# Optimization experiments

Hardware: AMD Instinct MI355X
Metric: run time of the kernel (lower is better)

## Reference

```python
import jax, jax.numpy as jnp
import numpy as np

B, D, H, W, C = 2, 6, 64, 64, 192
NH = 8                      # num heads
HD = C // NH                # head dim
E, K, HID = 8, 2, 384       # experts, top_k, d_hidden
WS = (2, 8, 8)              # window size (Wd, Wh, Ww)
SS = (1, 4, 4)              # shift size
N = WS[0] * WS[1] * WS[2]   # 128 tokens per window
NW = (D // WS[0]) * (H // WS[1]) * (W // WS[2])  # 192 windows per sample
SCALE = HD ** -0.5


def _rel_pos_index():
    coords = np.stack(np.meshgrid(np.arange(WS[0]), np.arange(WS[1]), np.arange(WS[2]), indexing='ij'))
    coords = coords.reshape(3, -1)
    rel = (coords[:, :, None] - coords[:, None, :]).transpose(1, 2, 0).astype(np.int64)
    rel[..., 0] += WS[0] - 1
    rel[..., 1] += WS[1] - 1
    rel[..., 2] += WS[2] - 1
    rel[..., 0] *= (2 * WS[1] - 1) * (2 * WS[2] - 1)
    rel[..., 1] *= (2 * WS[2] - 1)
    return rel.sum(-1)  # (N, N)


def _sine_pos_encoding():
    # VRT get_sine_position_encoding(window_size[1:], dim//2, normalize=True)
    h, w, nf = WS[1], WS[2], C // 2
    scale = 2 * np.pi
    y = np.cumsum(np.ones((1, h, w)), 1)
    x = np.cumsum(np.ones((1, h, w)), 2)
    y = y / (y[:, -1:, :] + 1e-6) * scale
    x = x / (x[:, :, -1:] + 1e-6) * scale
    dim_t = 10000.0 ** (2 * (np.arange(nf) // 2) / nf)
    px = x[..., None] / dim_t
    py = y[..., None] / dim_t
    px = np.stack([np.sin(px[..., 0::2]), np.cos(px[..., 1::2])], -1).reshape(1, h, w, -1)
    py = np.stack([np.sin(py[..., 0::2]), np.cos(py[..., 1::2])], -1).reshape(1, h, w, -1)
    return np.concatenate([py, px], -1).reshape(1, h * w, C).astype(np.float32)


def _compute_mask():
    # VRT compute_mask for cyclic shift
    img = np.zeros((1, D, H, W, 1))
    cnt = 0
    for d in (slice(0, -WS[0]), slice(-WS[0], -SS[0]), slice(-SS[0], None)):
        for h in (slice(0, -WS[1]), slice(-WS[1], -SS[1]), slice(-SS[1], None)):
            for w in (slice(0, -WS[2]), slice(-WS[2], -SS[2]), slice(-SS[2], None)):
                img[:, d, h, w, :] = cnt
                cnt += 1
    mw = img.reshape(1, D // WS[0], WS[0], H // WS[1], WS[1], W // WS[2], WS[2], 1)
    mw = mw.transpose(0, 1, 3, 5, 2, 4, 6, 7).reshape(-1, N)
    am = mw[:, None, :] - mw[:, :, None]
    return np.where(am != 0, -100.0, 0.0).astype(np.float32)  # (NW, N, N)


RP_INDEX = jnp.asarray(_rel_pos_index())
POS_BIAS = jnp.asarray(_sine_pos_encoding())  # (1, Wh*Ww, C)


def layernorm(x, w, b):
    mu = x.mean(-1, keepdims=True)
    var = ((x - mu) ** 2).mean(-1, keepdims=True)
    return (x - mu) * jax.lax.rsqrt(var + 1e-5) * w + b


def window_partition(x):
    x = x.reshape(B, D // WS[0], WS[0], H // WS[1], WS[1], W // WS[2], WS[2], C)
    return x.transpose(0, 1, 3, 5, 2, 4, 6, 7).reshape(-1, N, C)


def window_reverse(wx):
    x = wx.reshape(B, D // WS[0], H // WS[1], W // WS[2], WS[0], WS[1], WS[2], C)
    return x.transpose(0, 1, 4, 2, 5, 3, 6, 7).reshape(B, D, H, W, C)


def _attn(q, k, v, mask, bias):
    # q,k,v: (B_, NH, n, HD); mask: (NW, N, N) or None; bias: (NH, n, n) or None
    n = q.shape[2]
    a = jnp.einsum('bhnd,bhmd->bhnm', q * SCALE, k)
    if bias is not None:
        a = a + bias[None]
    if mask is not None:
        a = a.reshape(-1, NW, NH, n, n) + mask[None, :, None, :n, :n]
        a = a.reshape(-1, NH, n, n)
    a = jax.nn.softmax(a, -1)
    o = jnp.einsum('bhnm,bhmd->bhnd', a, v)
    return o.transpose(0, 2, 1, 3).reshape(o.shape[0], n, NH * HD)


def reference(x, mask_matrix, n1_w, n1_b, qkv_self_w, qkv_self_b, qkv_mut_w, qkv_mut_b,
              rpb_table, proj_w, proj_b, n2_w, n2_b, gate_w, gate_b, W1, b1, W2, b2):
    # ---- part 1: shifted 3D window attention (self + mutual) ----
    xn = layernorm(x, n1_w, n1_b)
    xs = jnp.roll(xn, shift=(-SS[0], -SS[1], -SS[2]), axis=(1, 2, 3))
    xw = window_partition(xs)  # (B_, N, C)
    B_ = xw.shape[0]

    def qkv_split(t):
        t = t.reshape(B_, -1, 3, NH, HD).transpose(2, 0, 3, 1, 4)
        return t[0], t[1], t[2]

    # self attention with relative position bias
    q, k, v = qkv_split(xw @ qkv_self_w + qkv_self_b)
    bias = rpb_table[RP_INDEX.reshape(-1)].reshape(N, N, NH).transpose(2, 0, 1)
    x_self = _attn(q, k, v, mask_matrix, bias)

    # mutual attention between the two frames of each window
    xm = xw + jnp.tile(POS_BIAS, (1, 2, 1))
    q, k, v = qkv_split(xm @ qkv_mut_w + qkv_mut_b)
    half = N // 2
    q1, q2 = q[:, :, :half], q[:, :, half:]
    k1, k2 = k[:, :, :half], k[:, :, half:]
    v1, v2 = v[:, :, :half], v[:, :, half:]
    x1 = _attn(q2, k1, v1, mask_matrix, None)
    x2 = _attn(q1, k2, v2, mask_matrix, None)
    x_out = jnp.concatenate([jnp.concatenate([x1, x2], 1), x_self], 2)  # (B_, N, 2C)

    attn_out = x_out @ proj_w + proj_b  # (B_, N, C)
    xr = window_reverse(attn_out)
    xr = jnp.roll(xr, shift=SS, axis=(1, 2, 3))
    x = x + xr

    # ---- part 2: MoE FFN (top-2 gate, per-expert 2-layer MLP, weighted combine) ----
    xn = layernorm(x, n2_w, n2_b).reshape(-1, C)  # (T, C)
    logits = xn @ gate_w + gate_b  # (T, E)
    top_val, top_idx = jax.lax.top_k(logits, K)
    scores = jax.nn.softmax(top_val, -1)  # (T, K)
    cw = (jax.nn.one_hot(top_idx, E, dtype=xn.dtype) * scores[..., None]).sum(1)  # (T, E)

    def body(acc, p):
        w1, bb1, w2, bb2, cwe = p
        hdd = jax.nn.gelu(xn @ w1 + bb1, approximate=False)
        return acc + cwe[:, None] * (hdd @ w2 + bb2), None

    moe_out, _ = jax.lax.scan(body, jnp.zeros_like(xn), (W1, b1, W2, b2, cw.T))
    return x + moe_out.reshape(B, D, H, W, C)


def setup_inputs() -> dict:
    key = jax.random.key(0)
    ks = jax.random.split(key, 8)
    s = 0.02
    tbl = (2 * WS[0] - 1) * (2 * WS[1] - 1) * (2 * WS[2] - 1)
    return dict(
        x=jax.random.normal(ks[0], (B, D, H, W, C), jnp.float32),
        mask_matrix=jnp.asarray(_compute_mask()),
        n1_w=jnp.ones((C,), jnp.float32), n1_b=jnp.zeros((C,), jnp.float32),
        qkv_self_w=jax.random.normal(ks[1], (C, 3 * C), jnp.float32) * s,
        qkv_self_b=jnp.zeros((3 * C,), jnp.float32),
        qkv_mut_w=jax.random.normal(ks[2], (C, 3 * C), jnp.float32) * s,
        qkv_mut_b=jnp.zeros((3 * C,), jnp.float32),
        rpb_table=jax.random.normal(ks[3], (tbl, NH), jnp.float32) * s,
        proj_w=jax.random.normal(ks[4], (2 * C, C), jnp.float32) * s,
        proj_b=jnp.zeros((C,), jnp.float32),
        n2_w=jnp.ones((C,), jnp.float32), n2_b=jnp.zeros((C,), jnp.float32),
        gate_w=jax.random.normal(ks[5], (C, E), jnp.float32) * s,
        gate_b=jnp.zeros((E,), jnp.float32),
        W1=jax.random.normal(ks[6], (E, C, HID), jnp.float32) * s,
        b1=jnp.zeros((E, HID), jnp.float32),
        W2=jax.random.normal(ks[7], (E, HID, C), jnp.float32) * s,
        b2=jnp.zeros((E, C), jnp.float32),
    )
```

## Files before the change

kernel.cpp:

```cpp
#include <hip/hip_runtime.h>
#include <hip/hip_bf16.h>

#define NW_ 192
#define NWIN 384
#define NTOK 128
#define CC 192
#define NHD 8
#define HD 24
#define QKVC 576
#define NROWS 49152
#define HIDN 384
#define SCALE_Q 0.20412414523193154f

typedef __hip_bfloat16 bf16;
typedef __attribute__((ext_vector_type(8))) short s16x8;
typedef __attribute__((ext_vector_type(4))) float f32x4;

__device__ __forceinline__ float waveRedSum(float v) {
    v += __shfl_xor(v, 32);
    v += __shfl_xor(v, 16);
    v += __shfl_xor(v, 8);
    v += __shfl_xor(v, 4);
    v += __shfl_xor(v, 2);
    v += __shfl_xor(v, 1);
    return v;
}

__device__ __forceinline__ size_t row_to_x(int r) {
    int wb = r >> 7;
    int n = r & 127;
    int b = wb / NW_;
    int rem = wb % NW_;
    int wd = rem >> 6;
    int wh = (rem >> 3) & 7;
    int ww = rem & 7;
    int id = n >> 6;
    int ih = (n >> 3) & 7;
    int iw = n & 7;
    int d = (wd * 2 + id + 1) % 6;
    int h = (wh * 8 + ih + 4) & 63;
    int w = (ww * 8 + iw + 4) & 63;
    return ((size_t)((b * 6 + d) * 64 + h) * 64 + w) * CC;
}

__device__ __forceinline__ void split_store(float v, bf16* hi, bf16* lo) {
    bf16 h = __float2bfloat16(v);
    *hi = h;
    *lo = __float2bfloat16(v - __bfloat162float(h));
}

__global__ void zero_counts(int* counts) {
    if (threadIdx.x < 8) counts[threadIdx.x] = 0;
}

__global__ __launch_bounds__(256) void transpose_w(
    const float* __restrict__ in, bf16* __restrict__ out_hi,
    bf16* __restrict__ out_lo, int K, int N) {
    size_t total = (size_t)K * N;
    in += (size_t)blockIdx.z * total;
    out_hi += (size_t)blockIdx.z * total;
    int t = blockIdx.x * 256 + threadIdx.x;
    if (t >= (int)total) return;
    int n = t / K, k = t % K;
    float v = in[(size_t)k * N + n];
    bf16 h = __float2bfloat16(v);
    out_hi[t] = h;
    if (out_lo) {
        out_lo += (size_t)blockIdx.z * total;
        out_lo[t] = __float2bfloat16(v - __bfloat162float(h));
    }
}

__global__ __launch_bounds__(256) void build_rpbx(
    const float* __restrict__ rpb, float* __restrict__ rpbx) {
    int idx = blockIdx.x * 256 + threadIdx.x;
    int q = idx >> 7, k = idx & 127;
    int dn = q >> 6, hn = (q >> 3) & 7, wn = q & 7;
    int dm = k >> 6, hm = (k >> 3) & 7, wm = k & 7;
    int ridx = (dn - dm + 1) * 225 + (hn - hm + 7) * 15 + (wn - wm + 7);
#pragma unroll
    for (int h = 0; h < 8; ++h)
        rpbx[h * 16384 + idx] = rpb[ridx * 8 + h];
}

__global__ __launch_bounds__(256) void ln1_partition(
    const float* __restrict__ x, const float* __restrict__ n1w,
    const float* __restrict__ n1b, bf16* __restrict__ xw_hi,
    bf16* __restrict__ xw_lo) {
    int r = blockIdx.x * 4 + (threadIdx.x >> 6);
    int t = threadIdx.x & 63;
    const float* src = x + row_to_x(r);
    float v0 = src[t], v1 = src[t + 64], v2 = src[t + 128];
    float mu = waveRedSum(v0 + v1 + v2) * (1.0f / 192.0f);
    float d0 = v0 - mu, d1 = v1 - mu, d2 = v2 - mu;
    float var = waveRedSum(d0 * d0 + d1 * d1 + d2 * d2) * (1.0f / 192.0f);
    float rstd = rsqrtf(var + 1e-5f);
    size_t b = (size_t)r * CC;
    split_store(d0 * rstd * n1w[t]       + n1b[t],       xw_hi + b + t,       xw_lo + b + t);
    split_store(d1 * rstd * n1w[t + 64]  + n1b[t + 64],  xw_hi + b + t + 64,  xw_lo + b + t + 64);
    split_store(d2 * rstd * n1w[t + 128] + n1b[t + 128], xw_hi + b + t + 128, xw_lo + b + t + 128);
}

__global__ __launch_bounds__(256) void add_posbias(
    bf16* __restrict__ hi, bf16* __restrict__ lo) {
    int idx = blockIdx.x * 256 + threadIdx.x;
    if (idx >= NROWS * CC) return;
    int c = idx % CC;
    int r = idx / CC;
    int n = r & 127;
    int tkn = n & 63;
    int h = tkn >> 3, w = tkn & 7;
    const float twopi_over = 6.283185307179586f / (8.0f + 1e-6f);
    float coord = (c < 96) ? (h + 1) * twopi_over : (w + 1) * twopi_over;
    int cc = (c < 96) ? c : c - 96;
    int j = cc >> 1;
    float v = coord * __expf(-0.1918820910968785f * (float)j);
    float pe = (cc & 1) ? __cosf(v) : __sinf(v);
    float val = __bfloat162float(hi[idx]) + __bfloat162float(lo[idx]) + pe;
    split_store(val, hi + idx, lo + idx);
}

template <int EPI, int GSHIFT, bool GATHER, bool SPLIT>
__global__ __launch_bounds__(256) void mgemm(
    const bf16* __restrict__ A, const bf16* __restrict__ Alo, int ldA,
    const bf16* __restrict__ Wt, const bf16* __restrict__ Wtlo, int wStrideE,
    const float* __restrict__ bias, int biasStrideE,
    float* __restrict__ Cf, bf16* __restrict__ Cb,
    int M, int K, int N,
    const int* __restrict__ counts, const int* __restrict__ lists,
    const float* __restrict__ wts, const float* __restrict__ xres) {
    int e = blockIdx.z;
    int Mq = counts ? counts[e] : M;
    int bm = blockIdx.x * 64;
    if (bm >= Mq) return;
    int bn = blockIdx.y * 64;
    const int lbase = e * NROWS;
    __shared__ __align__(16) bf16 As[64][72];
    __shared__ __align__(16) bf16 Bs[64][72];
    __shared__ __align__(16) bf16 Asl[(SPLIT ? 64 : 1)][72];
    __shared__ __align__(16) bf16 Bsl[(SPLIT ? 64 : 1)][72];
    int t = threadIdx.x;
    int trow = t >> 2, tko = (t & 3) * 8;
    size_t aoff;
    if (GATHER) {
        int p = bm + trow;
        int a = lists[lbase + (p < Mq ? p : 0)];
        aoff = (size_t)(a >> GSHIFT) * (size_t)ldA + tko;
    } else {
        aoff = (size_t)(bm + trow) * (size_t)ldA + tko;
    }
    size_t boff = (size_t)e * wStrideE + (size_t)(bn + trow) * K + tko;
    int wv = t >> 6, l = t & 63;
    int fr = l & 15, fg = l >> 4;
    f32x4 acc[4] = {{0.f,0.f,0.f,0.f},{0.f,0.f,0.f,0.f},
                    {0.f,0.f,0.f,0.f},{0.f,0.f,0.f,0.f}};
    for (int k0 = 0; k0 < K; k0 += 64) {
        __syncthreads();
        *(int4*)&As[trow][tko]      = *(const int4*)(A + aoff + k0);
        *(int4*)&As[trow][tko + 32] = *(const int4*)(A + aoff + k0 + 32);
        *(int4*)&Bs[trow][tko]      = *(const int4*)(Wt + boff + k0);
        *(int4*)&Bs[trow][tko + 32] = *(const int4*)(Wt + boff + k0 + 32);
        if (SPLIT) {
            *(int4*)&Asl[trow][tko]      = *(const int4*)(Alo + aoff + k0);
            *(int4*)&Asl[trow][tko + 32] = *(const int4*)(Alo + aoff + k0 + 32);
            *(int4*)&Bsl[trow][tko]      = *(const int4*)(Wtlo + boff + k0);
            *(int4*)&Bsl[trow][tko + 32] = *(const int4*)(Wtlo + boff + k0 + 32);
        }
        __syncthreads();
#pragma unroll
        for (int ks = 0; ks < 2; ++ks) {
            s16x8 ah = *(const s16x8*)&As[wv * 16 + fr][ks * 32 + fg * 8];
            s16x8 al;
            if (SPLIT) al = *(const s16x8*)&Asl[wv * 16 + fr][ks * 32 + fg * 8];
#pragma unroll
            for (int nt = 0; nt < 4; ++nt) {
                s16x8 bh = *(const s16x8*)&Bs[nt * 16 + fr][ks * 32 + fg * 8];
                acc[nt] = __builtin_amdgcn_mfma_f32_16x16x32_bf16(ah, bh, acc[nt], 0, 0, 0);
                if (SPLIT) {
                    s16x8 bl = *(const s16x8*)&Bsl[nt * 16 + fr][ks * 32 + fg * 8];
                    acc[nt] = __builtin_amdgcn_mfma_f32_16x16x32_bf16(ah, bl, acc[nt], 0, 0, 0);
                    acc[nt] = __builtin_amdgcn_mfma_f32_16x16x32_bf16(al, bh, acc[nt], 0, 0, 0);
                }
            }
        }
    }
    int row0 = bm + wv * 16 + fg * 4;
    if (EPI == 0) {
#pragma unroll
        for (int nt = 0; nt < 4; ++nt) {
            int c = bn + nt * 16 + fr;
            float bv = bias[c];
#pragma unroll
            for (int i = 0; i < 4; ++i)
                Cf[(size_t)(row0 + i) * N + c] = acc[nt][i] + bv;
        }
    } else if (EPI == 1) {
        size_t sr[4];
#pragma unroll
        for (int i = 0; i < 4; ++i) sr[i] = row_to_x(row0 + i);
#pragma unroll
        for (int nt = 0; nt < 4; ++nt) {
            int c = bn + nt * 16 + fr;
            float bv = bias[c];
#pragma unroll
            for (int i = 0; i < 4; ++i)
                Cf[sr[i] + c] = xres[sr[i] + c] + acc[nt][i] + bv;
        }
    } else if (EPI == 2) {
        const float* bp = bias + (size_t)e * biasStrideE;
#pragma unroll
        for (int i = 0; i < 4; ++i) {
            int p = row0 + i;
            if (p < Mq) {
                int a = lists[lbase + p];
#pragma unroll
                for (int nt = 0; nt < 4; ++nt) {
                    int c = bn + nt * 16 + fr;
                    float v = acc[nt][i] + bp[c];
                    float g = 0.5f * v * (1.0f + erff(v * 0.7071067811865476f));
                    Cb[(size_t)a * HIDN + c] = __float2bfloat16(g);
                }
            }
        }
    } else if (EPI == 3) {
        const float* bp = bias + (size_t)e * biasStrideE;
#pragma unroll
        for (int i = 0; i < 4; ++i) {
            int p = row0 + i;
            if (p < Mq) {
                int a = lists[lbase + p];
                int r = a >> 1;
                float w = wts[lbase + p];
#pragma unroll
                for (int nt = 0; nt < 4; ++nt) {
                    int c = bn + nt * 16 + fr;
                    atomicAdd(&Cf[(size_t)r * CC + c], w * (acc[nt][i] + bp[c]));
                }
            }
        }
    } else {
        const size_t S0 = (size_t)NROWS * 192;
        const size_t S1 = (size_t)NROWS * 24;
#pragma unroll
        for (int nt = 0; nt < 4; ++nt) {
            int c = bn + nt * 16 + fr;
            int which = c / 192;
            int rem = c - which * 192;
            int hh = rem / 24;
            int d = rem - hh * 24;
            float bv = bias[c];
            bf16* hb = Cb + (size_t)(2 * which) * S0 + (size_t)hh * S1;
            bf16* lb = Cb + (size_t)(2 * which + 1) * S0 + (size_t)hh * S1;
#pragma unroll
            for (int i = 0; i < 4; ++i) {
                float v = acc[nt][i] + bv;
                if (which == 0) v *= SCALE_Q;
                size_t o = (size_t)(row0 + i) * 24 + d;
                split_store(v, hb + o, lb + o);
            }
        }
    }
}

template <bool SELF>
__global__ __launch_bounds__(256) void attn_mfma(
    const bf16* __restrict__ qkvp, const float* __restrict__ mask,
    const float* __restrict__ rpbx, bf16* __restrict__ cat_hi,
    bf16* __restrict__ cat_lo) {
    constexpr int NT = SELF ? 128 : 64;
    constexpr int KT = NT / 16;
    constexpr int CPW = NT / 64;
    constexpr int KS = NT / 32;
    const size_t S0 = (size_t)NROWS * 192;
    const size_t S1 = (size_t)NROWS * 24;

    int wb = blockIdx.x, hh = blockIdx.y;
    int hf = SELF ? 0 : blockIdx.z;
    int qbase = wb * NTOK + (SELF ? 0 : (hf ? 0 : 64));
    int kvbase = wb * NTOK + (SELF ? 0 : (hf ? 64 : 0));
    int t = threadIdx.x;
    int wv = t >> 6, l = t & 63, fr = l & 15, fg = l >> 4;

    __shared__ __align__(16) ushort Vth[32][144];
    __shared__ __align__(16) ushort Vtl[32][144];
    __shared__ float linv_s[NT];

    {
        constexpr int PPT = 256 / NT;
        constexpr int DP = 24 / PPT;
        int tok = t % NT;
        int part = t / NT;
        const ushort* vh = (const ushort*)(qkvp + 4 * S0) + hh * S1 +
                           (size_t)(kvbase + tok) * 24 + part * DP;
        const ushort* vl = (const ushort*)(qkvp + 5 * S0) + hh * S1 +
                           (size_t)(kvbase + tok) * 24 + part * DP;
#pragma unroll
        for (int u = 0; u < DP; ++u) {
            Vth[part * DP + u][tok] = vh[u];
            Vtl[part * DP + u][tok] = vl[u];
        }
    }

    s16x8 zf = {0, 0, 0, 0, 0, 0, 0, 0};
    f32x4 st[KT][CPW];
#pragma unroll
    for (int kt = 0; kt < KT; ++kt)
#pragma unroll
        for (int c = 0; c < CPW; ++c) st[kt][c] = (f32x4){0.f, 0.f, 0.f, 0.f};

    s16x8 qfh[CPW], qfl[CPW];
#pragma unroll
    for (int c = 0; c < CPW; ++c) {
        int qt = wv * CPW + c;
        const bf16* qrow = qkvp + hh * S1 + (size_t)(qbase + qt * 16 + fr) * 24 + fg * 8;
        qfh[c] = (fg < 3) ? *(const s16x8*)qrow : zf;
        qfl[c] = (fg < 3) ? *(const s16x8*)(qrow + S0) : zf;
    }
#pragma unroll
    for (int kt = 0; kt < KT; ++kt) {
        const bf16* krow = qkvp + 2 * S0 + hh * S1 + (size_t)(kvbase + kt * 16 + fr) * 24 + fg * 8;
        s16x8 kh = (fg < 3) ? *(const s16x8*)krow : zf;
        s16x8 kl = (fg < 3) ? *(const s16x8*)(krow + S0) : zf;
#pragma unroll
        for (int c = 0; c < CPW; ++c) {
            st[kt][c] = __builtin_amdgcn_mfma_f32_16x16x32_bf16(kh, qfh[c], st[kt][c], 0, 0, 0);
            st[kt][c] = __builtin_amdgcn_mfma_f32_16x16x32_bf16(kh, qfl[c], st[kt][c], 0, 0, 0);
            st[kt][c] = __builtin_amdgcn_mfma_f32_16x16x32_bf16(kl, qfh[c], st[kt][c], 0, 0, 0);
        }
    }

    uint phq[KT][CPW][2], plq[KT][CPW][2];
#pragma unroll
    for (int c = 0; c < CPW; ++c) {
        int q = (wv * CPW + c) * 16 + fr;
        const float* mrow = mask + ((size_t)(wb % NW_) * NTOK + q) * NTOK;
        const float* brow = rpbx + ((size_t)hh * NTOK + q) * NTOK;
        float mx = -1e30f;
#pragma unroll
        for (int kt = 0; kt < KT; ++kt) {
            int k0 = kt * 16 + fg * 4;
            float4 mk = *(const float4*)(mrow + k0);
            if (SELF) {
                float4 bs = *(const float4*)(brow + k0);
                mk.x += bs.x; mk.y += bs.y; mk.z += bs.z; mk.w += bs.w;
            }
            st[kt][c][0] += mk.x; st[kt][c][1] += mk.y;
            st[kt][c][2] += mk.z; st[kt][c][3] += mk.w;
#pragma unroll
            for (int i = 0; i < 4; ++i) mx = fmaxf(mx, st[kt][c][i]);
        }
        mx = fmaxf(mx, __shfl_xor(mx, 16));
        mx = fmaxf(mx, __shfl_xor(mx, 32));
        float ls = 0.f;
#pragma unroll
        for (int kt = 0; kt < KT; ++kt)
#pragma unroll
            for (int i = 0; i < 4; ++i) {
                float pv = __expf(st[kt][c][i] - mx);
                st[kt][c][i] = pv;
                ls += pv;
            }
        ls += __shfl_xor(ls, 16);
        ls += __shfl_xor(ls, 32);
        if (fg == 0) linv_s[q] = 1.0f / ls;
#pragma unroll
        for (int kt = 0; kt < KT; ++kt) {
            ushort hb[4], lb[4];
#pragma unroll
            for (int i = 0; i < 4; ++i) {
                float pv = st[kt][c][i];
                bf16 ph = __float2bfloat16(pv);
                hb[i] = *(ushort*)&ph;
                bf16 pl = __float2bfloat16(pv - __bfloat162float(ph));
                lb[i] = *(ushort*)&pl;
            }
            phq[kt][c][0] = (uint)hb[0] | ((uint)hb[1] << 16);
            phq[kt][c][1] = (uint)hb[2] | ((uint)hb[3] << 16);
            plq[kt][c][0] = (uint)lb[0] | ((uint)lb[1] << 16);
            plq[kt][c][1] = (uint)lb[2] | ((uint)lb[3] << 16);
        }
    }
    __syncthreads();

    f32x4 oacc[CPW][2];
#pragma unroll
    for (int rt = 0; rt < CPW; ++rt)
#pragma unroll
        for (int ct = 0; ct < 2; ++ct) oacc[rt][ct] = (f32x4){0.f, 0.f, 0.f, 0.f};

    int sA = fr + 32 * (fg & 1);
    int sB = sA + 16;
    bool tsel = fg >= 2;
#pragma unroll
    for (int ks = 0; ks < KS; ++ks) {
        s16x8 bh[2], bl[2];
#pragma unroll
        for (int ct = 0; ct < 2; ++ct) {
            bh[ct] = *(const s16x8*)&Vth[ct * 16 + fr][ks * 32 + fg * 8];
            bl[ct] = *(const s16x8*)&Vtl[ct * 16 + fr][ks * 32 + fg * 8];
        }
#pragma unroll
        for (int rt = 0; rt < CPW; ++rt) {
            union { uint u[4]; s16x8 v; } ah, al;
            uint x0, x1;
            x0 = __shfl(phq[2 * ks][rt][0], sA); x1 = __shfl(phq[2 * ks + 1][rt][0], sA);
            ah.u[0] = tsel ? x1 : x0;
            x0 = __shfl(phq[2 * ks][rt][1], sA); x1 = __shfl(phq[2 * ks + 1][rt][1], sA);
            ah.u[1] = tsel ? x1 : x0;
            x0 = __shfl(phq[2 * ks][rt][0], sB); x1 = __shfl(phq[2 * ks + 1][rt][0], sB);
            ah.u[2] = tsel ? x1 : x0;
            x0 = __shfl(phq[2 * ks][rt][1], sB); x1 = __shfl(phq[2 * ks + 1][rt][1], sB);
            ah.u[3] = tsel ? x1 : x0;
            x0 = __shfl(plq[2 * ks][rt][0], sA); x1 = __shfl(plq[2 * ks + 1][rt][0], sA);
            al.u[0] = tsel ? x1 : x0;
            x0 = __shfl(plq[2 * ks][rt][1], sA); x1 = __shfl(plq[2 * ks + 1][rt][1], sA);
            al.u[1] = tsel ? x1 : x0;
            x0 = __shfl(plq[2 * ks][rt][0], sB); x1 = __shfl(plq[2 * ks + 1][rt][0], sB);
            al.u[2] = tsel ? x1 : x0;
            x0 = __shfl(plq[2 * ks][rt][1], sB); x1 = __shfl(plq[2 * ks + 1][rt][1], sB);
            al.u[3] = tsel ? x1 : x0;
#pragma unroll
            for (int ct = 0; ct < 2; ++ct) {
                oacc[rt][ct] = __builtin_amdgcn_mfma_f32_16x16x32_bf16(ah.v, bh[ct], oacc[rt][ct], 0, 0, 0);
                oacc[rt][ct] = __builtin_amdgcn_mfma_f32_16x16x32_bf16(ah.v, bl[ct], oacc[rt][ct], 0, 0, 0);
                oacc[rt][ct] = __builtin_amdgcn_mfma_f32_16x16x32_bf16(al.v, bh[ct], oacc[rt][ct], 0, 0, 0);
            }
        }
    }

#pragma unroll
    for (int rt = 0; rt < CPW; ++rt)
#pragma unroll
        for (int ct = 0; ct < 2; ++ct) {
            int d = ct * 16 + fr;
            if (d < 24) {
#pragma unroll
                for (int i = 0; i < 4; ++i) {
                    int q = (wv * CPW + rt) * 16 + fg * 4 + i;
                    float val = oacc[rt][ct][i] * linv_s[q];
                    int otok = SELF ? q : (hf ? 64 + q : q);
                    size_t ob = (size_t)(wb * NTOK + otok) * 384 + (SELF ? 192 : 0) + hh * 24 + d;
                    split_store(val, cat_hi + ob, cat_lo + ob);
                }
            }
        }
}

__global__ __launch_bounds__(256) void ln2_gate(
    const float* __restrict__ xin, const float* __restrict__ n2w,
    const float* __restrict__ n2b, const float* __restrict__ gw,
    const float* __restrict__ gb, bf16* __restrict__ xn2,
    uchar2* __restrict__ ee, float2* __restrict__ ww) {
    __shared__ float sh[4][192];
    int wave = threadIdx.x >> 6;
    int t = threadIdx.x & 63;
    int r = blockIdx.x * 4 + wave;
    const float* src = xin + (size_t)r * CC;
    float v0 = src[t], v1 = src[t + 64], v2 = src[t + 128];
    float mu = waveRedSum(v0 + v1 + v2) * (1.0f / 192.0f);
    float d0 = v0 - mu, d1 = v1 - mu, d2 = v2 - mu;
    float var = waveRedSum(d0 * d0 + d1 * d1 + d2 * d2) * (1.0f / 192.0f);
    float rstd = rsqrtf(var + 1e-5f);
    float o0 = d0 * rstd * n2w[t] + n2b[t];
    float o1 = d1 * rstd * n2w[t + 64] + n2b[t + 64];
    float o2 = d2 * rstd * n2w[t + 128] + n2b[t + 128];
    bf16* dst = xn2 + (size_t)r * CC;
    dst[t] = __float2bfloat16(o0);
    dst[t + 64] = __float2bfloat16(o1);
    dst[t + 128] = __float2bfloat16(o2);
    sh[wave][t] = o0; sh[wave][t + 64] = o1; sh[wave][t + 128] = o2;
    __builtin_amdgcn_wave_barrier();
    int e = t & 7, ch = t >> 3;
    float part = 0.0f;
    for (int c = ch * 24; c < ch * 24 + 24; ++c) part += sh[wave][c] * gw[c * 8 + e];
    part += __shfl_xor(part, 8);
    part += __shfl_xor(part, 16);
    part += __shfl_xor(part, 32);
    float logit = part + gb[e];
    float b1v = -1e30f, b2v = -1e30f;
    int i1 = 0, i2 = 0;
    for (int qe = 0; qe < 8; ++qe) {
        float lv = __shfl(logit, qe);
        if (lv > b1v) { b2v = b1v; i2 = i1; b1v = lv; i1 = qe; }
        else if (lv > b2v) { b2v = lv; i2 = qe; }
    }
    if (t == 0) {
        float e2 = __expf(b2v - b1v);
        float inv = 1.0f / (1.0f + e2);
        ee[r] = make_uchar2((unsigned char)i1, (unsigned char)i2);
        ww[r] = make_float2(inv, e2 * inv);
    }
}

__global__ __launch_bounds__(256) void route(
    const uchar2* __restrict__ ee, const float2* __restrict__ ww,
    int* __restrict__ counts, int* __restrict__ lists, float* __restrict__ wts) {
    __shared__ int lcnt[8];
    __shared__ int lbase[8];
    int t = threadIdx.x;
    int r = blockIdx.x * 256 + t;
    if (t < 8) lcnt[t] = 0;
    __syncthreads();
    uchar2 e = ee[r];
    float2 w = ww[r];
    int p1 = atomicAdd(&lcnt[e.x], 1);
    int p2 = atomicAdd(&lcnt[e.y], 1);
    __syncthreads();
    if (t < 8) lbase[t] = atomicAdd(&counts[t], lcnt[t]);
    __syncthreads();
    int d1 = e.x * NROWS + lbase[e.x] + p1;
    int d2 = e.y * NROWS + lbase[e.y] + p2;
    lists[d1] = r * 2;
    wts[d1] = w.x;
    lists[d2] = r * 2 + 1;
    wts[d2] = w.y;
}

extern "C" void kernel_launch(void* const* d_in, const int* in_sizes, int n_in,
                              void* d_out, int out_size, void* d_ws, size_t ws_size,
                              hipStream_t stream) {
    const float* x     = (const float*)d_in[0];
    const float* mask  = (const float*)d_in[1];
    const float* n1w   = (const float*)d_in[2];
    const float* n1b   = (const float*)d_in[3];
    const float* qkvsw = (const float*)d_in[4];
    const float* qkvsb = (const float*)d_in[5];
    const float* qkvmw = (const float*)d_in[6];
    const float* qkvmb = (const float*)d_in[7];
    const float* rpb   = (const float*)d_in[8];
    const float* projw = (const float*)d_in[9];
    const float* projb = (const float*)d_in[10];
    const float* n2w   = (const float*)d_in[11];
    const float* n2b   = (const float*)d_in[12];
    const float* gw    = (const float*)d_in[13];
    const float* gb    = (const float*)d_in[14];
    const float* W1    = (const float*)d_in[15];
    const float* b1    = (const float*)d_in[16];
    const float* W2    = (const float*)d_in[17];
    const float* b2    = (const float*)d_in[18];
    float* out = (float*)d_out;
    const size_t S0 = (size_t)NROWS * 192;

    char* p = (char*)d_ws;
    bf16* xw_hi = (bf16*)p;     p += S0 * 2;
    bf16* xw_lo = (bf16*)p;     p += S0 * 2;
    bf16* qkvp = (bf16*)p;
    bf16* H = (bf16*)p;         p += S0 * 6 * 2;
    bf16* cat_hi = (bf16*)p;    p += (size_t)NROWS * 384 * 2;
    bf16* cat_lo = (bf16*)p;    p += (size_t)NROWS * 384 * 2;
    bf16* xn2 = (bf16*)p;       p += S0 * 2;
    int* counts = (int*)p;      p += 32;
    int* lists = (int*)p;       p += (size_t)8 * NROWS * 4;
    float* wts = (float*)p;     p += (size_t)8 * NROWS * 4;
    uchar2* ee = (uchar2*)p;    p += (size_t)NROWS * 2;
    float2* ww = (float2*)p;    p += (size_t)NROWS * 8;
    float* rpbx = (float*)p;    p += (size_t)8 * 16384 * 4;
    bf16* qkvswT_hi = (bf16*)p; p += 110592 * 2;
    bf16* qkvswT_lo = (bf16*)p; p += 110592 * 2;
    bf16* qkvmwT_hi = (bf16*)p; p += 110592 * 2;
    bf16* qkvmwT_lo = (bf16*)p; p += 110592 * 2;
    bf16* projwT_hi = (bf16*)p; p += 73728 * 2;
    bf16* projwT_lo = (bf16*)p; p += 73728 * 2;
    bf16* W1T = (bf16*)p;       p += (size_t)8 * 73728 * 2;
    bf16* W2T = (bf16*)p;       p += (size_t)8 * 73728 * 2;

    zero_counts<<<1, 64, 0, stream>>>(counts);
    build_rpbx<<<64, 256, 0, stream>>>(rpb, rpbx);
    transpose_w<<<dim3(432, 1, 1), 256, 0, stream>>>(qkvsw, qkvswT_hi, qkvswT_lo, 192, 576);
    transpose_w<<<dim3(432, 1, 1), 256, 0, stream>>>(qkvmw, qkvmwT_hi, qkvmwT_lo, 192, 576);
    transpose_w<<<dim3(288, 1, 1), 256, 0, stream>>>(projw, projwT_hi, projwT_lo, 384, 192);
    transpose_w<<<dim3(288, 1, 8), 256, 0, stream>>>(W1, W1T, nullptr, 192, 384);
    transpose_w<<<dim3(288, 1, 8), 256, 0, stream>>>(W2, W2T, nullptr, 384, 192);

    ln1_partition<<<NROWS / 4, 256, 0, stream>>>(x, n1w, n1b, xw_hi, xw_lo);
    mgemm<4, 0, false, true><<<dim3(768, 9, 1), 256, 0, stream>>>(
        xw_hi, xw_lo, CC, qkvswT_hi, qkvswT_lo, 0, qkvsb, 0, nullptr, qkvp,
        NROWS, CC, QKVC, nullptr, nullptr, nullptr, nullptr);
    attn_mfma<true><<<dim3(NWIN, NHD), 256, 0, stream>>>(qkvp, mask, rpbx, cat_hi, cat_lo);
    add_posbias<<<(NROWS * CC) / 256, 256, 0, stream>>>(xw_hi, xw_lo);
    mgemm<4, 0, false, true><<<dim3(768, 9, 1), 256, 0, stream>>>(
        xw_hi, xw_lo, CC, qkvmwT_hi, qkvmwT_lo, 0, qkvmb, 0, nullptr, qkvp,
        NROWS, CC, QKVC, nullptr, nullptr, nullptr, nullptr);
    attn_mfma<false><<<dim3(NWIN, NHD, 2), 256, 0, stream>>>(qkvp, mask, rpbx, cat_hi, cat_lo);
    mgemm<1, 0, false, true><<<dim3(768, 3, 1), 256, 0, stream>>>(
        cat_hi, cat_lo, 384, projwT_hi, projwT_lo, 0, projb, 0, out, nullptr,
        NROWS, 384, CC, nullptr, nullptr, nullptr, x);
    ln2_gate<<<NROWS / 4, 256, 0, stream>>>(out, n2w, n2b, gw, gb, xn2, ee, ww);
    route<<<NROWS / 256, 256, 0, stream>>>(ee, ww, counts, lists, wts);
    mgemm<2, 1, true, false><<<dim3(768, 6, 8), 256, 0, stream>>>(
        xn2, nullptr, CC, W1T, nullptr, 73728, b1, HIDN, nullptr, H,
        NROWS, CC, HIDN, counts, lists, nullptr, nullptr);
    mgemm<3, 0, true, false><<<dim3(768, 3, 8), 256, 0, stream>>>(
        H, nullptr, HIDN, W2T, nullptr, 73728, b2, CC, out, nullptr,
        NROWS, HIDN, CC, counts, lists, wts, nullptr);
}
```

Measured before the change: 694.9 us.

## Enlarge GEMM block tile to 128x64 with 2x2 wave register tiling

The shared GEMM kernel moves from a 64x64 block tile, where each wave computes 16x64, to a 128x64 tile where each wave computes a 64x32 sub-tile (4x2 MFMA fragments). Each B fragment is now reused across four A fragments, which cuts LDS reads per MFMA and halves the number of blocks and weight-tile reloads. In exchange it uses more accumulator and fragment registers, which may lower occupancy, and shared memory grows to roughly 55KB for the split-precision variant. The gathered MoE GEMMs also waste more work on their partial last tiles.

```diff
diff --git a/kernel.cpp b/kernel.cpp
--- a/kernel.cpp
+++ b/kernel.cpp
@@ -131,132 +131,150 @@
     const float* __restrict__ wts, const float* __restrict__ xres) {
     int e = blockIdx.z;
     int Mq = counts ? counts[e] : M;
-    int bm = blockIdx.x * 64;
+    int bm = blockIdx.x * 128;
     if (bm >= Mq) return;
     int bn = blockIdx.y * 64;
     const int lbase = e * NROWS;
-    __shared__ __align__(16) bf16 As[64][72];
+    __shared__ __align__(16) bf16 As[128][72];
     __shared__ __align__(16) bf16 Bs[64][72];
-    __shared__ __align__(16) bf16 Asl[(SPLIT ? 64 : 1)][72];
+    __shared__ __align__(16) bf16 Asl[(SPLIT ? 128 : 1)][72];
     __shared__ __align__(16) bf16 Bsl[(SPLIT ? 64 : 1)][72];
     int t = threadIdx.x;
-    int trow = t >> 2, tko = (t & 3) * 8;
+    int arow = t >> 1, acol = (t & 1) * 32;
+    int brow = t >> 2, bcol = (t & 3) * 16;
     size_t aoff;
     if (GATHER) {
-        int p = bm + trow;
+        int p = bm + arow;
         int a = lists[lbase + (p < Mq ? p : 0)];
-        aoff = (size_t)(a >> GSHIFT) * (size_t)ldA + tko;
+        aoff = (size_t)(a >> GSHIFT) * (size_t)ldA + acol;
     } else {
-        aoff = (size_t)(bm + trow) * (size_t)ldA + tko;
-    }
-    size_t boff = (size_t)e * wStrideE + (size_t)(bn + trow) * K + tko;
+        aoff = (size_t)(bm + arow) * (size_t)ldA + acol;
+    }
+    size_t boff = (size_t)e * wStrideE + (size_t)(bn + brow) * K + bcol;
     int wv = t >> 6, l = t & 63;
+    int wvm = wv >> 1, wvn = wv & 1;
     int fr = l & 15, fg = l >> 4;
-    f32x4 acc[4] = {{0.f,0.f,0.f,0.f},{0.f,0.f,0.f,0.f},
-                    {0.f,0.f,0.f,0.f},{0.f,0.f,0.f,0.f}};
+    f32x4 acc[4][2];
+#pragma unroll
+    for (int mf = 0; mf < 4; ++mf)
+#pragma unroll
+        for (int nf = 0; nf < 2; ++nf) acc[mf][nf] = (f32x4){0.f, 0.f, 0.f, 0.f};
     for (int k0 = 0; k0 < K; k0 += 64) {
         __syncthreads();
-        *(int4*)&As[trow][tko]      = *(const int4*)(A + aoff + k0);
-        *(int4*)&As[trow][tko + 32] = *(const int4*)(A + aoff + k0 + 32);
-        *(int4*)&Bs[trow][tko]      = *(const int4*)(Wt + boff + k0);
-        *(int4*)&Bs[trow][tko + 32] = *(const int4*)(Wt + boff + k0 + 32);
+#pragma unroll
+        for (int u = 0; u < 4; ++u)
+            *(int4*)&As[arow][acol + u * 8] = *(const int4*)(A + aoff + k0 + u * 8);
+        *(int4*)&Bs[brow][bcol]     = *(const int4*)(Wt + boff + k0);
+        *(int4*)&Bs[brow][bcol + 8] = *(const int4*)(Wt + boff + k0 + 8);
         if (SPLIT) {
-            *(int4*)&Asl[trow][tko]      = *(const int4*)(Alo + aoff + k0);
-            *(int4*)&Asl[trow][tko + 32] = *(const int4*)(Alo + aoff + k0 + 32);
-            *(int4*)&Bsl[trow][tko]      = *(const int4*)(Wtlo + boff + k0);
-            *(int4*)&Bsl[trow][tko + 32] = *(const int4*)(Wtlo + boff + k0 + 32);
+#pragma unroll
+            for (int u = 0; u < 4; ++u)
+                *(int4*)&Asl[arow][acol + u * 8] = *(const int4*)(Alo + aoff + k0 + u * 8);
+            *(int4*)&Bsl[brow][bcol]     = *(const int4*)(Wtlo + boff + k0);
+            *(int4*)&Bsl[brow][bcol + 8] = *(const int4*)(Wtlo + boff + k0 + 8);
         }
         __syncthreads();
 #pragma unroll
         for (int ks = 0; ks < 2; ++ks) {
-            s16x8 ah = *(const s16x8*)&As[wv * 16 + fr][ks * 32 + fg * 8];
-            s16x8 al;
-            if (SPLIT) al = *(const s16x8*)&Asl[wv * 16 + fr][ks * 32 + fg * 8];
-#pragma unroll
-            for (int nt = 0; nt < 4; ++nt) {
-                s16x8 bh = *(const s16x8*)&Bs[nt * 16 + fr][ks * 32 + fg * 8];
-                acc[nt] = __builtin_amdgcn_mfma_f32_16x16x32_bf16(ah, bh, acc[nt], 0, 0, 0);
-                if (SPLIT) {
-                    s16x8 bl = *(const s16x8*)&Bsl[nt * 16 + fr][ks * 32 + fg * 8];
-                    acc[nt] = __builtin_amdgcn_mfma_f32_16x16x32_bf16(ah, bl, acc[nt], 0, 0, 0);
-                    acc[nt] = __builtin_amdgcn_mfma_f32_16x16x32_bf16(al, bh, acc[nt], 0, 0, 0);
+            s16x8 ah[4], al[4], bh[2], bl[2];
+#pragma unroll
+            for (int mf = 0; mf < 4; ++mf) {
+                ah[mf] = *(const s16x8*)&As[wvm * 64 + mf * 16 + fr][ks * 32 + fg * 8];
+                if (SPLIT) al[mf] = *(const s16x8*)&Asl[wvm * 64 + mf * 16 + fr][ks * 32 + fg * 8];
+            }
+#pragma unroll
+            for (int nf = 0; nf < 2; ++nf) {
+                bh[nf] = *(const s16x8*)&Bs[wvn * 32 + nf * 16 + fr][ks * 32 + fg * 8];
+                if (SPLIT) bl[nf] = *(const s16x8*)&Bsl[wvn * 32 + nf * 16 + fr][ks * 32 + fg * 8];
+            }
+#pragma unroll
+            for (int mf = 0; mf < 4; ++mf)
+#pragma unroll
+                for (int nf = 0; nf < 2; ++nf) {
+                    acc[mf][nf] = __builtin_amdgcn_mfma_f32_16x16x32_bf16(ah[mf], bh[nf], acc[mf][nf], 0, 0, 0);
+                    if (SPLIT) {
+                        acc[mf][nf] = __builtin_amdgcn_mfma_f32_16x16x32_bf16(ah[mf], bl[nf], acc[mf][nf], 0, 0, 0);
+                        acc[mf][nf] = __builtin_amdgcn_mfma_f32_16x16x32_bf16(al[mf], bh[nf], acc[mf][nf], 0, 0, 0);
+                    }
                 }
-            }
-        }
-    }
-    int row0 = bm + wv * 16 + fg * 4;
-    if (EPI == 0) {
-#pragma unroll
-        for (int nt = 0; nt < 4; ++nt) {
-            int c = bn + nt * 16 + fr;
-            float bv = bias[c];
-#pragma unroll
-            for (int i = 0; i < 4; ++i)
-                Cf[(size_t)(row0 + i) * N + c] = acc[nt][i] + bv;
-        }
-    } else if (EPI == 1) {
-        size_t sr[4];
-#pragma unroll
-        for (int i = 0; i < 4; ++i) sr[i] = row_to_x(row0 + i);
-#pragma unroll
-        for (int nt = 0; nt < 4; ++nt) {
-            int c = bn + nt * 16 + fr;
-            float bv = bias[c];
-#pragma unroll
-            for (int i = 0; i < 4; ++i)
-                Cf[sr[i] + c] = xres[sr[i] + c] + acc[nt][i] + bv;
-        }
-    } else if (EPI == 2) {
-        const float* bp = bias + (size_t)e * biasStrideE;
-#pragma unroll
-        for (int i = 0; i < 4; ++i) {
-            int p = row0 + i;
-            if (p < Mq) {
-                int a = lists[lbase + p];
-#pragma unroll
-                for (int nt = 0; nt < 4; ++nt) {
-                    int c = bn + nt * 16 + fr;
-                    float v = acc[nt][i] + bp[c];
-                    float g = 0.5f * v * (1.0f + erff(v * 0.7071067811865476f));
-                    Cb[(size_t)a * HIDN + c] = __float2bfloat16(g);
+        }
+    }
+#pragma unroll
+    for (int mf = 0; mf < 4; ++mf) {
+        int row0 = bm + wvm * 64 + mf * 16 + fg * 4;
+        if (EPI == 0) {
+#pragma unroll
+            for (int nf = 0; nf < 2; ++nf) {
+                int c = bn + wvn * 32 + nf * 16 + fr;
+                float bv = bias[c];
+#pragma unroll
+                for (int i = 0; i < 4; ++i)
+                    Cf[(size_t)(row0 + i) * N + c] = acc[mf][nf][i] + bv;
+            }
+        } else if (EPI == 1) {
+            size_t sr[4];
+#pragma unroll
+            for (int i = 0; i < 4; ++i) sr[i] = row_to_x(row0 + i);
+#pragma unroll
+            for (int nf = 0; nf < 2; ++nf) {
+                int c = bn + wvn * 32 + nf * 16 + fr;
+                float bv = bias[c];
+#pragma unroll
+                for (int i = 0; i < 4; ++i)
+                    Cf[sr[i] + c] = xres[sr[i] + c] + acc[mf][nf][i] + bv;
+            }
+        } else if (EPI == 2) {
+            const float* bp = bias + (size_t)e * biasStrideE;
+#pragma unroll
+            for (int i = 0; i < 4; ++i) {
+                int p = row0 + i;
+                if (p < Mq) {
+                    int a = lists[lbase + p];
+#pragma unroll
+                    for (int nf = 0; nf < 2; ++nf) {
+                        int c = bn + wvn * 32 + nf * 16 + fr;
+                        float v = acc[mf][nf][i] + bp[c];
+                        float g = 0.5f * v * (1.0f + erff(v * 0.7071067811865476f));
+                        Cb[(size_t)a * HIDN + c] = __float2bfloat16(g);
+                    }
                 }
             }
-        }
-    } else if (EPI == 3) {
-        const float* bp = bias + (size_t)e * biasStrideE;
-#pragma unroll
-        for (int i = 0; i < 4; ++i) {
-            int p = row0 + i;
-            if (p < Mq) {
-                int a = lists[lbase + p];
-                int r = a >> 1;
-                float w = wts[lbase + p];
-#pragma unroll
-                for (int nt = 0; nt < 4; ++nt) {
-                    int c = bn + nt * 16 + fr;
-                    atomicAdd(&Cf[(size_t)r * CC + c], w * (acc[nt][i] + bp[c]));
+        } else if (EPI == 3) {
+            const float* bp = bias + (size_t)e * biasStrideE;
+#pragma unroll
+            for (int i = 0; i < 4; ++i) {
+                int p = row0 + i;
+                if (p < Mq) {
+                    int a = lists[lbase + p];
+                    int r = a >> 1;
+                    float w = wts[lbase + p];
+#pragma unroll
+                    for (int nf = 0; nf < 2; ++nf) {
+                        int c = bn + wvn * 32 + nf * 16 + fr;
+                        atomicAdd(&Cf[(size_t)r * CC + c], w * (acc[mf][nf][i] + bp[c]));
+                    }
                 }
             }
-        }
-    } else {
-        const size_t S0 = (size_t)NROWS * 192;
-        const size_t S1 = (size_t)NROWS * 24;
-#pragma unroll
-        for (int nt = 0; nt < 4; ++nt) {
-            int c = bn + nt * 16 + fr;
-            int which = c / 192;
-            int rem = c - which * 192;
-            int hh = rem / 24;
-            int d = rem - hh * 24;
-            float bv = bias[c];
-            bf16* hb = Cb + (size_t)(2 * which) * S0 + (size_t)hh * S1;
-            bf16* lb = Cb + (size_t)(2 * which + 1) * S0 + (size_t)hh * S1;
-#pragma unroll
-            for (int i = 0; i < 4; ++i) {
-                float v = acc[nt][i] + bv;
-                if (which == 0) v *= SCALE_Q;
-                size_t o = (size_t)(row0 + i) * 24 + d;
-                split_store(v, hb + o, lb + o);
+        } else {
+            const size_t S0 = (size_t)NROWS * 192;
+            const size_t S1 = (size_t)NROWS * 24;
+#pragma unroll
+            for (int nf = 0; nf < 2; ++nf) {
+                int c = bn + wvn * 32 + nf * 16 + fr;
+                int which = c / 192;
+                int rem = c - which * 192;
+                int hh = rem / 24;
+                int d = rem - hh * 24;
+                float bv = bias[c];
+                bf16* hb = Cb + (size_t)(2 * which) * S0 + (size_t)hh * S1;
+                bf16* lb = Cb + (size_t)(2 * which + 1) * S0 + (size_t)hh * S1;
+#pragma unroll
+                for (int i = 0; i < 4; ++i) {
+                    float v = acc[mf][nf][i] + bv;
+                    if (which == 0) v *= SCALE_Q;
+                    size_t o = (size_t)(row0 + i) * 24 + d;
+                    split_store(v, hb + o, lb + o);
+                }
             }
         }
     }
@@ -573,24 +591,24 @@
     transpose_w<<<dim3(288, 1, 8), 256, 0, stream>>>(W2, W2T, nullptr, 384, 192);
 
     ln1_partition<<<NROWS / 4, 256, 0, stream>>>(x, n1w, n1b, xw_hi, xw_lo);
-    mgemm<4, 0, false, true><<<dim3(768, 9, 1), 256, 0, stream>>>(
+    mgemm<4, 0, false, true><<<dim3(384, 9, 1), 256, 0, stream>>>(
         xw_hi, xw_lo, CC, qkvswT_hi, qkvswT_lo, 0, qkvsb, 0, nullptr, qkvp,
         NROWS, CC, QKVC, nullptr, nullptr, nullptr, nullptr);
     attn_mfma<true><<<dim3(NWIN, NHD), 256, 0, stream>>>(qkvp, mask, rpbx, cat_hi, cat_lo);
     add_posbias<<<(NROWS * CC) / 256, 256, 0, stream>>>(xw_hi, xw_lo);
-    mgemm<4, 0, false, true><<<dim3(768, 9, 1), 256, 0, stream>>>(
+    mgemm<4, 0, false, true><<<dim3(384, 9, 1), 256, 0, stream>>>(
         xw_hi, xw_lo, CC, qkvmwT_hi, qkvmwT_lo, 0, qkvmb, 0, nullptr, qkvp,
         NROWS, CC, QKVC, nullptr, nullptr, nullptr, nullptr);
     attn_mfma<false><<<dim3(NWIN, NHD, 2), 256, 0, stream>>>(qkvp, mask, rpbx, cat_hi, cat_lo);
-    mgemm<1, 0, false, true><<<dim3(768, 3, 1), 256, 0, stream>>>(
+    mgemm<1, 0, false, true><<<dim3(384, 3, 1), 256, 0, stream>>>(
         cat_hi, cat_lo, 384, projwT_hi, projwT_lo, 0, projb, 0, out, nullptr,
         NROWS, 384, CC, nullptr, nullptr, nullptr, x);
     ln2_gate<<<NROWS / 4, 256, 0, stream>>>(out, n2w, n2b, gw, gb, xn2, ee, ww);
     route<<<NROWS / 256, 256, 0, stream>>>(ee, ww, counts, lists, wts);
-    mgemm<2, 1, true, false><<<dim3(768, 6, 8), 256, 0, stream>>>(
+    mgemm<2, 1, true, false><<<dim3(384, 6, 8), 256, 0, stream>>>(
         xn2, nullptr, CC, W1T, nullptr, 73728, b1, HIDN, nullptr, H,
         NROWS, CC, HIDN, counts, lists, nullptr, nullptr);
-    mgemm<3, 0, true, false><<<dim3(768, 3, 8), 256, 0, stream>>>(
+    mgemm<3, 0, true, false><<<dim3(384, 3, 8), 256, 0, stream>>>(
         H, nullptr, HIDN, W2T, nullptr, 73728, b2, CC, out, nullptr,
         NROWS, HIDN, CC, counts, lists, wts, nullptr);
 }
```

New measurement: 701.4 us. Within noise of the previous version (+0.9%).
